# Optimization experiments

Hardware: AMD Instinct MI355X
Metric: run time of the kernel (lower is better)

## Reference

```python
import jax, jax.numpy as jnp
import numpy as np

HEADS = 8
EPS = 1e-5

def setup_inputs() -> dict:
    key = jax.random.key(0)
    ks = jax.random.split(key, 4)
    B, S, N, C = 1, 256, 384, 512
    msa = jax.random.normal(ks[0], (B, S, N, C), dtype=jnp.float32)
    mask = jnp.ones((B, S), dtype=jnp.int32)
    Wqkv = jax.random.normal(ks[1], (3 * C, C), dtype=jnp.float32) * (C ** -0.5)
    bqkv = jnp.zeros((3 * C,), dtype=jnp.float32)
    Wout = jax.random.normal(ks[2], (C, C), dtype=jnp.float32) * (C ** -0.5)
    bout = jnp.zeros((C,), dtype=jnp.float32)
    gamma = jnp.ones((C,), dtype=jnp.float32)
    beta = jnp.zeros((C,), dtype=jnp.float32)
    return {"msa": msa, "mask": mask, "Wqkv": Wqkv, "bqkv": bqkv,
            "Wout": Wout, "bout": bout, "gamma": gamma, "beta": beta}

def reference(msa, mask, Wqkv, bqkv, Wout, bout, gamma, beta):
    B, S, N, C = msa.shape
    H = HEADS
    Dh = C // H
    scale = Dh ** -0.5
    msa_t = jnp.transpose(msa, (0, 2, 1, 3))            # [B,N,S,C]
    qkv = msa_t @ Wqkv.T + bqkv                          # [B,N,S,3C]
    qkv = qkv.reshape(B, N, S, 3, H, Dh)
    q, k, v = qkv[..., 0, :, :], qkv[..., 1, :, :], qkv[..., 2, :, :]  # [B,N,S,H,Dh]
    attn = jnp.einsum('bnshc,bnthc->bhst', q, k) * scale  # reduce over N and head-dim
    attn = jnp.where(mask[:, None, None, :] == 0, -1e9, attn)
    attn = jax.nn.softmax(attn, axis=-1)                 # [B,H,S,S]
    out = jnp.einsum('bhst,bnthc->bnshc', attn, v).reshape(B, N, S, C)
    out = jnp.transpose(out, (0, 2, 1, 3))               # [B,S,N,C]
    out = out @ Wout.T + bout
    x = msa + out
    mu = jnp.mean(x, axis=-1, keepdims=True)
    var = jnp.mean((x - mu) ** 2, axis=-1, keepdims=True)
    return (x - mu) * jax.lax.rsqrt(var + EPS) * gamma + beta
```

## Files before the change

kernel.cpp:

```cpp
#include <hip/hip_runtime.h>

#define S_ 256
#define N_ 384
#define C_ 512
#define H_ 8
#define R_ (N_*S_)
#define SPLITK 32
#define NPK (N_/SPLITK)

typedef _Float16 f16;
typedef _Float16 f16x8 __attribute__((ext_vector_type(8)));
typedef float f32x4 __attribute__((ext_vector_type(4)));

#define MFMA16(a,b,c) __builtin_amdgcn_mfma_f32_16x16x32_f16(a,b,c,0,0,0)

typedef __attribute__((address_space(3))) unsigned int as3_u32;
typedef __attribute__((address_space(1))) const unsigned int as1_u32;

__device__ __forceinline__ void gl_lds16(const void* g, void* l) {
    __builtin_amdgcn_global_load_lds((as1_u32*)(unsigned long long)g,
                                     (as3_u32*)(unsigned long long)l, 16, 0, 0);
}

__device__ __forceinline__ int swz_off(int row, int g) {
    return row*64 + (((g) ^ (row & 7)) << 3);
}

__device__ __forceinline__ void stage_tile32(const f16* __restrict__ Ab,
                                             const f16* __restrict__ Bb,
                                             int stride, f16* As_, f16* Bs_,
                                             int tid, int wid) {
#pragma unroll
    for (int i = 0; i < 2; ++i) {
        int id = (i << 8) + tid;
        int row = id >> 2;
        int g = (id & 3) ^ ((row >> 1) & 3);
        int lofs = ((i << 8) + (wid << 6)) << 4;
        gl_lds16(Ab + row * stride + (g << 3), (char*)As_ + lofs);
        gl_lds16(Bb + row * stride + (g << 3), (char*)Bs_ + lofs);
    }
}

__device__ __forceinline__ void frag_mma32(const f16* As_, const f16* Bs_,
                                           int lane, int wr, int wc, f32x4 acc[4][4]) {
    int kg = lane >> 4;
    f16x8 af[4], bf[4];
#pragma unroll
    for (int m = 0; m < 4; ++m) {
        int row = wr + (m << 4) + (lane & 15);
        af[m] = *(const f16x8*)&As_[row * 32 + ((kg ^ ((row >> 1) & 3)) << 3)];
    }
#pragma unroll
    for (int j = 0; j < 4; ++j) {
        int row = wc + (j << 4) + (lane & 15);
        bf[j] = *(const f16x8*)&Bs_[row * 32 + ((kg ^ ((row >> 1) & 3)) << 3)];
    }
#pragma unroll
    for (int m = 0; m < 4; ++m)
#pragma unroll
        for (int j = 0; j < 4; ++j)
            acc[m][j] = MFMA16(af[m], bf[j], acc[m][j]);
}

__device__ __forceinline__ void frag_mma64(const f16* As_, const f16* Bs_,
                                           int lane, int wr, int wc, f32x4 acc[4][4]) {
#pragma unroll
    for (int ks = 0; ks < 64; ks += 32) {
        int kg = (ks >> 3) + (lane >> 4);
        f16x8 af[4], bf[4];
#pragma unroll
        for (int m = 0; m < 4; ++m)
            af[m] = *(const f16x8*)&As_[swz_off(wr + (m << 4) + (lane & 15), kg)];
#pragma unroll
        for (int j = 0; j < 4; ++j)
            bf[j] = *(const f16x8*)&Bs_[swz_off(wc + (j << 4) + (lane & 15), kg)];
#pragma unroll
        for (int m = 0; m < 4; ++m)
#pragma unroll
            for (int j = 0; j < 4; ++j)
                acc[m][j] = MFMA16(af[m], bf[j], acc[m][j]);
    }
}

__global__ __launch_bounds__(256) void k_prep(const float* __restrict__ Wqkv,
                                              const float* __restrict__ Wout,
                                              f16* __restrict__ Wq16, f16* __restrict__ Wo16) {
    int i = blockIdx.x * 256 + threadIdx.x;
    if (i < 1536 * C_) Wq16[i] = (f16)Wqkv[i];
    if (i < C_ * C_)   Wo16[i] = (f16)Wout[i];
}

__global__ __launch_bounds__(256) void k_cast(const float* __restrict__ msa,
                                              f16* __restrict__ msaT) {
    int t = blockIdx.x * 256 + threadIdx.x;
    int r = t >> 6, cg = t & 63;
    int n = r >> 8, s = r & 255;
    const float* src = msa + (s * N_ + n) * C_ + (cg << 3);
    float4 lo = *(const float4*)src;
    float4 hi = *(const float4*)(src + 4);
    f16x8 v;
    v[0]=(f16)lo.x; v[1]=(f16)lo.y; v[2]=(f16)lo.z; v[3]=(f16)lo.w;
    v[4]=(f16)hi.x; v[5]=(f16)hi.y; v[6]=(f16)hi.z; v[7]=(f16)hi.w;
    *(f16x8*)(msaT + r * C_ + (cg << 3)) = v;
}

__global__ __launch_bounds__(256) void k_qkv(const f16* __restrict__ msaT,
                                             const f16* __restrict__ W,
                                             const float* __restrict__ bqkv,
                                             f16* __restrict__ qk,
                                             f16* __restrict__ vT) {
    int wg = (blockIdx.x & 7) * 1152 + (blockIdx.x >> 3);
    int bx = wg / 12, by = wg % 12;
    int j0 = by << 7;
    int tid = threadIdx.x, lane = tid & 63, wid = tid >> 6;
    int wr = (wid >> 1) << 6, wc = (wid & 1) << 6;
    __shared__ f16 SH[16384];
    const f16* Abase = msaT + (bx << 7) * C_;
    const f16* Bbase = W + j0 * C_;
    f32x4 acc[4][4] = {};
    stage_tile32(Abase, Bbase, C_, SH, SH + 8192, tid, wid);
    __syncthreads();
    for (int t = 0; t < 16; ++t) {
        int cur = t & 1;
        if (t < 15)
            stage_tile32(Abase + ((t + 1) << 5), Bbase + ((t + 1) << 5), C_,
                         SH + ((cur ^ 1) << 12), SH + 8192 + ((cur ^ 1) << 12), tid, wid);
        frag_mma32(SH + (cur << 12), SH + 8192 + (cur << 12), lane, wr, wc, acc);
        __syncthreads();
    }
    if (by < 8) {
#pragma unroll
        for (int p = 0; p < 2; ++p) {
            __syncthreads();
#pragma unroll
            for (int mm = 0; mm < 2; ++mm) {
                int m = 2 * p + mm;
                int rl = (m << 4) + ((lane >> 4) << 2);
                int lrow = (wr >> 1) + rl - (p << 5);
#pragma unroll
                for (int j = 0; j < 4; ++j) {
                    int col = wc + (j << 4) + (lane & 15);
                    float bv = bqkv[j0 + col];
#pragma unroll
                    for (int q = 0; q < 4; ++q)
                        SH[(lrow + q) * 136 + col] = (f16)(acc[m][j][q] + bv);
                }
            }
            __syncthreads();
#pragma unroll
            for (int i = 0; i < 4; ++i) {
                int u = tid + (i << 8);
                int lrow = u >> 4, seg = u & 15;
                int grow = (bx << 7) + ((lrow >> 5) << 6) + (p << 5) + (lrow & 31);
                *(f16x8*)(qk + grow * 1024 + j0 + (seg << 3)) =
                    *(const f16x8*)&SH[lrow * 136 + (seg << 3)];
            }
        }
    } else {
        int n = bx >> 1, t0g = (bx & 1) << 7;
#pragma unroll
        for (int p = 0; p < 2; ++p) {
            __syncthreads();
#pragma unroll
            for (int m = 0; m < 4; ++m) {
                int rl = wr + (m << 4) + ((lane >> 4) << 2);
#pragma unroll
                for (int jj = 0; jj < 2; ++jj) {
                    int j = 2 * p + jj;
                    int col = wc + (j << 4) + (lane & 15);
                    int lcol = (col & 31) + ((col >> 6) << 5);
                    float bv = bqkv[1024 + (by - 8) * 128 + col];
#pragma unroll
                    for (int q = 0; q < 4; ++q)
                        SH[lcol * 136 + rl + q] = (f16)(acc[m][j][q] + bv);
                }
            }
            __syncthreads();
#pragma unroll
            for (int i = 0; i < 4; ++i) {
                int u = tid + (i << 8);
                int lcol = u >> 4, seg = u & 15;
                int col = (lcol & 31) + (p << 5) + ((lcol >> 5) << 6);
                int jg = (by - 8) * 128 + col;
                *(f16x8*)(vT + ((n * H_ + (jg >> 6)) * 64 + (jg & 63)) * S_ + t0g + (seg << 3)) =
                    *(const f16x8*)&SH[lcol * 136 + (seg << 3)];
            }
        }
    }
}

__global__ __launch_bounds__(256) void k_logits(const f16* __restrict__ qk,
                                                float* __restrict__ logP) {
    int wg = (blockIdx.x & 7) * 128 + (blockIdx.x >> 3);
    int sk = wg >> 5, rem = wg & 31, h = rem >> 2, sb = (rem >> 1) & 1, tb = rem & 1;
    int s0 = sb << 7, t0 = tb << 7, n0 = sk * NPK;
    int tid = threadIdx.x, lane = tid & 63, wid = tid >> 6;
    int wr = (wid >> 1) << 6, wc = (wid & 1) << 6;
    __shared__ f16 SH[16384];
    const f16* Aroot = qk + s0 * 1024 + (h << 6);
    const f16* Broot = qk + t0 * 1024 + 512 + (h << 6);
    f32x4 acc[4][4] = {};
    stage_tile32(Aroot + n0 * S_ * 1024, Broot + n0 * S_ * 1024, 1024,
                 SH, SH + 8192, tid, wid);
    __syncthreads();
    for (int t = 0; t < 2 * NPK; ++t) {
        int cur = t & 1;
        if (t < 2 * NPK - 1) {
            int tn = t + 1;
            int n = n0 + (tn >> 1), dh = (tn & 1) << 5;
            stage_tile32(Aroot + n * S_ * 1024 + dh, Broot + n * S_ * 1024 + dh, 1024,
                         SH + ((cur ^ 1) << 12), SH + 8192 + ((cur ^ 1) << 12), tid, wid);
        }
        frag_mma32(SH + (cur << 12), SH + 8192 + (cur << 12), lane, wr, wc, acc);
        __syncthreads();
    }
#pragma unroll
    for (int m = 0; m < 4; ++m) {
        int rloc = wr + (m << 4) + ((lane >> 4) << 2);
#pragma unroll
        for (int j = 0; j < 4; ++j) {
            int tc = t0 + wc + (j << 4) + (lane & 15);
#pragma unroll
            for (int q = 0; q < 4; ++q)
                logP[((sk * H_ + h) * S_ + s0 + rloc + q) * S_ + tc] = acc[m][j][q];
        }
    }
}

__global__ __launch_bounds__(256) void k_softmax(const float* __restrict__ logP,
                                                 const int* __restrict__ mask,
                                                 f16* __restrict__ attn) {
    int hs = blockIdx.x;
    int t = threadIdx.x, lane = t & 63, wid = t >> 6;
    float v = 0.f;
#pragma unroll
    for (int sk = 0; sk < SPLITK; ++sk)
        v += logP[(sk * H_ * S_ + hs) * S_ + t];
    v *= 0.125f;
    if (mask[t] == 0) v = -1e9f;
    __shared__ float redm[4], reds[4];
    float m_ = v;
    for (int o = 32; o > 0; o >>= 1) m_ = fmaxf(m_, __shfl_xor(m_, o));
    if (lane == 0) redm[wid] = m_;
    __syncthreads();
    float bm = fmaxf(fmaxf(redm[0], redm[1]), fmaxf(redm[2], redm[3]));
    float e = __expf(v - bm);
    float s_ = e;
    for (int o = 32; o > 0; o >>= 1) s_ += __shfl_xor(s_, o);
    if (lane == 0) reds[wid] = s_;
    __syncthreads();
    float tot = reds[0] + reds[1] + reds[2] + reds[3];
    attn[hs * S_ + t] = (f16)(e / tot);
}

__global__ __launch_bounds__(256) void k_pv(const f16* __restrict__ attn,
                                            const f16* __restrict__ vT,
                                            f16* __restrict__ attn_out) {
    int n = blockIdx.x >> 3, h = blockIdx.x & 7;
    int tid = threadIdx.x, lane = tid & 63, wid = tid >> 6;
    __shared__ f16 SH[20480];
    f16* As_ = SH;
    f16* Bs_ = SH + 16384;
    f32x4 acc[4][4] = {};
    const f16* Ab = attn + h * S_ * S_;
    const f16* Bb = vT + (n * H_ + h) * 64 * S_;
    for (int tt = 0; tt < 4; ++tt) {
        int t0 = tt << 6;
        __syncthreads();
#pragma unroll
        for (int i = 0; i < 8; ++i) {
            int id = (i << 8) + tid;
            int row = id >> 3, g = (id & 7) ^ (row & 7);
            int lofs = ((i << 8) + (wid << 6)) << 4;
            gl_lds16(Ab + row * S_ + t0 + (g << 3), (char*)As_ + lofs);
        }
#pragma unroll
        for (int i = 0; i < 2; ++i) {
            int id = (i << 8) + tid;
            int row = id >> 3, g = (id & 7) ^ (row & 7);
            int lofs = ((i << 8) + (wid << 6)) << 4;
            gl_lds16(Bb + row * S_ + t0 + (g << 3), (char*)Bs_ + lofs);
        }
        __syncthreads();
        frag_mma64(As_, Bs_, lane, wid << 6, 0, acc);
    }
#pragma unroll
    for (int p = 0; p < 2; ++p) {
        __syncthreads();
#pragma unroll
        for (int mm = 0; mm < 2; ++mm) {
            int m = 2 * p + mm;
            int rl = ((m & 1) << 4) + ((lane >> 4) << 2);
            int lrow = (wid << 5) + rl;
#pragma unroll
            for (int j = 0; j < 4; ++j) {
                int d = (j << 4) + (lane & 15);
#pragma unroll
                for (int q = 0; q < 4; ++q)
                    SH[(lrow + q) * 72 + d] = (f16)acc[m][j][q];
            }
        }
        __syncthreads();
#pragma unroll
        for (int i = 0; i < 4; ++i) {
            int u = tid + (i << 8);
            int row = u >> 3, seg = u & 7;
            int s = ((row >> 5) << 6) + (p << 5) + (row & 31);
            *(f16x8*)(attn_out + (n * S_ + s) * C_ + (h << 6) + (seg << 3)) =
                *(const f16x8*)&SH[row * 72 + (seg << 3)];
        }
    }
}

__global__ __launch_bounds__(512) void k_out_ln(const f16* __restrict__ attn_out,
                                                const f16* __restrict__ Wo,
                                                const float* __restrict__ bout,
                                                const f16* __restrict__ msaT,
                                                const float* __restrict__ gamma,
                                                const float* __restrict__ beta,
                                                float* __restrict__ out) {
    int r0 = blockIdx.x << 6;
    int n = r0 >> 8, s0 = r0 & 255;
    int tid = threadIdx.x, lane = tid & 63, wid = tid >> 6;
    __shared__ f16 SH[36864];
    f16* As_ = SH;
    f16* Bs_ = SH + 4096;
    __shared__ float redS[8][64], redQ[8][64], muS[64], rsS[64];
    f32x4 acc[4][4] = {};
    for (int kt = 0; kt < 8; ++kt) {
        int c0 = kt << 6;
        __syncthreads();
        {
            int row = tid >> 3, g = (tid & 7) ^ (row & 7);
            int lofs = (wid << 6) << 4;
            gl_lds16(attn_out + (r0 + row) * C_ + c0 + (g << 3), (char*)As_ + lofs);
        }
#pragma unroll
        for (int i = 0; i < 8; ++i) {
            int id = (i << 9) + tid;
            int row = id >> 3, g = (id & 7) ^ (row & 7);
            int lofs = ((i << 9) + (wid << 6)) << 4;
            gl_lds16(Wo + row * C_ + c0 + (g << 3), (char*)Bs_ + lofs);
        }
        __syncthreads();
        frag_mma64(As_, Bs_, lane, 0, wid << 6, acc);
    }
    float psum[4][4] = {}, psq[4][4] = {};
#pragma unroll
    for (int m = 0; m < 4; ++m)
#pragma unroll
        for (int j = 0; j < 4; ++j) {
            int c = (wid << 6) + (j << 4) + (lane & 15);
            float bj = bout[c];
#pragma unroll
            for (int q = 0; q < 4; ++q) {
                int rl = (m << 4) + ((lane >> 4) << 2) + q;
                float x = acc[m][j][q] + bj + (float)msaT[(r0 + rl) * C_ + c];
                acc[m][j][q] = x;
                psum[m][q] += x;
                psq[m][q] += x * x;
            }
        }
#pragma unroll
    for (int m = 0; m < 4; ++m)
#pragma unroll
        for (int q = 0; q < 4; ++q)
            for (int o = 1; o < 16; o <<= 1) {
                psum[m][q] += __shfl_xor(psum[m][q], o);
                psq[m][q]  += __shfl_xor(psq[m][q], o);
            }
    if ((lane & 15) == 0) {
#pragma unroll
        for (int m = 0; m < 4; ++m)
#pragma unroll
            for (int q = 0; q < 4; ++q) {
                int rl = (m << 4) + ((lane >> 4) << 2) + q;
                redS[wid][rl] = psum[m][q];
                redQ[wid][rl] = psq[m][q];
            }
    }
    __syncthreads();
    if (tid < 64) {
        float t1 = 0.f, t2 = 0.f;
#pragma unroll
        for (int w = 0; w < 8; ++w) { t1 += redS[w][tid]; t2 += redQ[w][tid]; }
        float mu = t1 * (1.0f / 512.0f);
        float var = t2 * (1.0f / 512.0f) - mu * mu;
        muS[tid] = mu;
        rsS[tid] = rsqrtf(var + 1e-5f);
    }
    __syncthreads();
#pragma unroll
    for (int m = 0; m < 4; ++m)
#pragma unroll
        for (int j = 0; j < 4; ++j) {
            int c = (wid << 6) + (j << 4) + (lane & 15);
            float g = gamma[c], bb = beta[c];
#pragma unroll
            for (int q = 0; q < 4; ++q) {
                int rl = (m << 4) + ((lane >> 4) << 2) + q;
                int s = s0 + rl;
                float y = (acc[m][j][q] - muS[rl]) * rsS[rl] * g + bb;
                out[(s * N_ + n) * C_ + c] = y;
            }
        }
}

extern "C" void kernel_launch(void* const* d_in, const int* in_sizes, int n_in,
                              void* d_out, int out_size, void* d_ws, size_t ws_size,
                              hipStream_t stream) {
    const float* msa   = (const float*)d_in[0];
    const int*   mask  = (const int*)d_in[1];
    const float* Wqkv  = (const float*)d_in[2];
    const float* bqkv  = (const float*)d_in[3];
    const float* Wout  = (const float*)d_in[4];
    const float* bout  = (const float*)d_in[5];
    const float* gamma = (const float*)d_in[6];
    const float* beta  = (const float*)d_in[7];
    float* out = (float*)d_out;
    char* ws = (char*)d_ws;

    f16*   qk   = (f16*)(ws);
    f16*   vT   = (f16*)(ws + 201326592);
    f16*   msaT = (f16*)(ws + 301989888);
    f16*   attn = (f16*)(ws + 402653184);
    f16*   Wq16 = (f16*)(ws + 403701760);
    f16*   Wo16 = (f16*)(ws + 405274624);
    float* logP = out;
    f16*   attn_out = qk;

    k_prep<<<dim3(3072), dim3(256), 0, stream>>>(Wqkv, Wout, Wq16, Wo16);
    k_cast<<<dim3(24576), dim3(256), 0, stream>>>(msa, msaT);
    k_qkv<<<dim3(9216), dim3(256), 0, stream>>>(msaT, Wq16, bqkv, qk, vT);
    k_logits<<<dim3(1024), dim3(256), 0, stream>>>(qk, logP);
    k_softmax<<<dim3(2048), dim3(256), 0, stream>>>(logP, mask, attn);
    k_pv<<<dim3(3072), dim3(256), 0, stream>>>(attn, vT, attn_out);
    k_out_ln<<<dim3(1536), dim3(512), 0, stream>>>(attn_out, Wo16, bout, msaT, gamma, beta, out);
}
```

Measured before the change: 628.5 us.

## Use 512-thread blocks and BK=64 tiles in QKV and logits GEMMs

```diff
diff --git a/kernel.cpp b/kernel.cpp
--- a/kernel.cpp
+++ b/kernel.cpp
@@ -26,40 +26,38 @@
     return row*64 + (((g) ^ (row & 7)) << 3);
 }
 
-__device__ __forceinline__ void stage_tile32(const f16* __restrict__ Ab,
-                                             const f16* __restrict__ Bb,
-                                             int stride, f16* As_, f16* Bs_,
-                                             int tid, int wid) {
+__device__ __forceinline__ void stage8(const f16* __restrict__ Ab,
+                                       const f16* __restrict__ Bb,
+                                       int stride, f16* As_, f16* Bs_,
+                                       int tid, int wid) {
 #pragma unroll
     for (int i = 0; i < 2; ++i) {
-        int id = (i << 8) + tid;
-        int row = id >> 2;
-        int g = (id & 3) ^ ((row >> 1) & 3);
-        int lofs = ((i << 8) + (wid << 6)) << 4;
+        int id = (i << 9) + tid;
+        int row = id >> 3, g = (id & 7) ^ (row & 7);
+        int lofs = ((i << 9) + (wid << 6)) << 4;
         gl_lds16(Ab + row * stride + (g << 3), (char*)As_ + lofs);
         gl_lds16(Bb + row * stride + (g << 3), (char*)Bs_ + lofs);
     }
 }
 
-__device__ __forceinline__ void frag_mma32(const f16* As_, const f16* Bs_,
-                                           int lane, int wr, int wc, f32x4 acc[4][4]) {
-    int kg = lane >> 4;
-    f16x8 af[4], bf[4];
-#pragma unroll
-    for (int m = 0; m < 4; ++m) {
-        int row = wr + (m << 4) + (lane & 15);
-        af[m] = *(const f16x8*)&As_[row * 32 + ((kg ^ ((row >> 1) & 3)) << 3)];
-    }
-#pragma unroll
-    for (int j = 0; j < 4; ++j) {
-        int row = wc + (j << 4) + (lane & 15);
-        bf[j] = *(const f16x8*)&Bs_[row * 32 + ((kg ^ ((row >> 1) & 3)) << 3)];
-    }
-#pragma unroll
-    for (int m = 0; m < 4; ++m)
-#pragma unroll
-        for (int j = 0; j < 4; ++j)
-            acc[m][j] = MFMA16(af[m], bf[j], acc[m][j]);
+__device__ __forceinline__ void mma8(const f16* As_, const f16* Bs_,
+                                     int lane, int wr, int wc, f32x4 acc[4][2]) {
+#pragma unroll
+    for (int ks = 0; ks < 64; ks += 32) {
+        int kg = (ks >> 3) + (lane >> 4);
+        f16x8 af[4], bf[2];
+#pragma unroll
+        for (int m = 0; m < 4; ++m)
+            af[m] = *(const f16x8*)&As_[swz_off(wr + (m << 4) + (lane & 15), kg)];
+#pragma unroll
+        for (int j = 0; j < 2; ++j)
+            bf[j] = *(const f16x8*)&Bs_[swz_off(wc + (j << 4) + (lane & 15), kg)];
+#pragma unroll
+        for (int m = 0; m < 4; ++m)
+#pragma unroll
+            for (int j = 0; j < 2; ++j)
+                acc[m][j] = MFMA16(af[m], bf[j], acc[m][j]);
+    }
 }
 
 __device__ __forceinline__ void frag_mma64(const f16* As_, const f16* Bs_,
@@ -104,7 +102,7 @@
     *(f16x8*)(msaT + r * C_ + (cg << 3)) = v;
 }
 
-__global__ __launch_bounds__(256) void k_qkv(const f16* __restrict__ msaT,
+__global__ __launch_bounds__(512) void k_qkv(const f16* __restrict__ msaT,
                                              const f16* __restrict__ W,
                                              const float* __restrict__ bqkv,
                                              f16* __restrict__ qk,
@@ -113,116 +111,101 @@
     int bx = wg / 12, by = wg % 12;
     int j0 = by << 7;
     int tid = threadIdx.x, lane = tid & 63, wid = tid >> 6;
-    int wr = (wid >> 1) << 6, wc = (wid & 1) << 6;
-    __shared__ f16 SH[16384];
+    int wr = (wid >> 2) << 6, wc = (wid & 3) << 5;
+    __shared__ f16 SH[32768];
     const f16* Abase = msaT + (bx << 7) * C_;
     const f16* Bbase = W + j0 * C_;
-    f32x4 acc[4][4] = {};
-    stage_tile32(Abase, Bbase, C_, SH, SH + 8192, tid, wid);
-    __syncthreads();
-    for (int t = 0; t < 16; ++t) {
-        int cur = t & 1;
-        if (t < 15)
-            stage_tile32(Abase + ((t + 1) << 5), Bbase + ((t + 1) << 5), C_,
-                         SH + ((cur ^ 1) << 12), SH + 8192 + ((cur ^ 1) << 12), tid, wid);
-        frag_mma32(SH + (cur << 12), SH + 8192 + (cur << 12), lane, wr, wc, acc);
+    f32x4 acc[4][2] = {};
+    stage8(Abase, Bbase, C_, SH, SH + 8192, tid, wid);
+    __syncthreads();
+    for (int kt = 0; kt < 8; ++kt) {
+        int cur = kt & 1;
+        if (kt < 7)
+            stage8(Abase + ((kt + 1) << 6), Bbase + ((kt + 1) << 6), C_,
+                   SH + ((cur ^ 1) << 14), SH + 8192 + ((cur ^ 1) << 14), tid, wid);
+        mma8(SH + (cur << 14), SH + 8192 + (cur << 14), lane, wr, wc, acc);
         __syncthreads();
     }
     if (by < 8) {
 #pragma unroll
-        for (int p = 0; p < 2; ++p) {
-            __syncthreads();
-#pragma unroll
-            for (int mm = 0; mm < 2; ++mm) {
-                int m = 2 * p + mm;
-                int rl = (m << 4) + ((lane >> 4) << 2);
-                int lrow = (wr >> 1) + rl - (p << 5);
-#pragma unroll
-                for (int j = 0; j < 4; ++j) {
-                    int col = wc + (j << 4) + (lane & 15);
-                    float bv = bqkv[j0 + col];
-#pragma unroll
-                    for (int q = 0; q < 4; ++q)
-                        SH[(lrow + q) * 136 + col] = (f16)(acc[m][j][q] + bv);
-                }
-            }
-            __syncthreads();
-#pragma unroll
-            for (int i = 0; i < 4; ++i) {
-                int u = tid + (i << 8);
-                int lrow = u >> 4, seg = u & 15;
-                int grow = (bx << 7) + ((lrow >> 5) << 6) + (p << 5) + (lrow & 31);
-                *(f16x8*)(qk + grow * 1024 + j0 + (seg << 3)) =
-                    *(const f16x8*)&SH[lrow * 136 + (seg << 3)];
-            }
+        for (int m = 0; m < 4; ++m) {
+            int rl = wr + (m << 4) + ((lane >> 4) << 2);
+#pragma unroll
+            for (int j = 0; j < 2; ++j) {
+                int col = wc + (j << 4) + (lane & 15);
+                float bv = bqkv[j0 + col];
+#pragma unroll
+                for (int q = 0; q < 4; ++q)
+                    SH[(rl + q) * 140 + col] = (f16)(acc[m][j][q] + bv);
+            }
+        }
+        __syncthreads();
+#pragma unroll
+        for (int i = 0; i < 4; ++i) {
+            int u = (i << 9) + tid;
+            int row = u >> 4, seg = u & 15;
+            *(f16x8*)(qk + ((bx << 7) + row) * 1024 + j0 + (seg << 3)) =
+                *(const f16x8*)&SH[row * 140 + (seg << 3)];
         }
     } else {
         int n = bx >> 1, t0g = (bx & 1) << 7;
 #pragma unroll
-        for (int p = 0; p < 2; ++p) {
-            __syncthreads();
-#pragma unroll
-            for (int m = 0; m < 4; ++m) {
-                int rl = wr + (m << 4) + ((lane >> 4) << 2);
-#pragma unroll
-                for (int jj = 0; jj < 2; ++jj) {
-                    int j = 2 * p + jj;
-                    int col = wc + (j << 4) + (lane & 15);
-                    int lcol = (col & 31) + ((col >> 6) << 5);
-                    float bv = bqkv[1024 + (by - 8) * 128 + col];
-#pragma unroll
-                    for (int q = 0; q < 4; ++q)
-                        SH[lcol * 136 + rl + q] = (f16)(acc[m][j][q] + bv);
-                }
-            }
-            __syncthreads();
-#pragma unroll
-            for (int i = 0; i < 4; ++i) {
-                int u = tid + (i << 8);
-                int lcol = u >> 4, seg = u & 15;
-                int col = (lcol & 31) + (p << 5) + ((lcol >> 5) << 6);
-                int jg = (by - 8) * 128 + col;
-                *(f16x8*)(vT + ((n * H_ + (jg >> 6)) * 64 + (jg & 63)) * S_ + t0g + (seg << 3)) =
-                    *(const f16x8*)&SH[lcol * 136 + (seg << 3)];
-            }
-        }
-    }
-}
-
-__global__ __launch_bounds__(256) void k_logits(const f16* __restrict__ qk,
+        for (int m = 0; m < 4; ++m) {
+            int rl = wr + (m << 4) + ((lane >> 4) << 2);
+#pragma unroll
+            for (int j = 0; j < 2; ++j) {
+                int col = wc + (j << 4) + (lane & 15);
+                float bv = bqkv[1024 + ((by - 8) << 7) + col];
+#pragma unroll
+                for (int q = 0; q < 4; ++q)
+                    SH[col * 140 + rl + q] = (f16)(acc[m][j][q] + bv);
+            }
+        }
+        __syncthreads();
+#pragma unroll
+        for (int i = 0; i < 4; ++i) {
+            int u = (i << 9) + tid;
+            int lcol = u >> 4, seg = u & 15;
+            int jg = ((by - 8) << 7) + lcol;
+            *(f16x8*)(vT + ((n * H_ + (jg >> 6)) * 64 + (jg & 63)) * S_ + t0g + (seg << 3)) =
+                *(const f16x8*)&SH[lcol * 140 + (seg << 3)];
+        }
+    }
+}
+
+__global__ __launch_bounds__(512) void k_logits(const f16* __restrict__ qk,
                                                 float* __restrict__ logP) {
     int wg = (blockIdx.x & 7) * 128 + (blockIdx.x >> 3);
     int sk = wg >> 5, rem = wg & 31, h = rem >> 2, sb = (rem >> 1) & 1, tb = rem & 1;
     int s0 = sb << 7, t0 = tb << 7, n0 = sk * NPK;
     int tid = threadIdx.x, lane = tid & 63, wid = tid >> 6;
-    int wr = (wid >> 1) << 6, wc = (wid & 1) << 6;
-    __shared__ f16 SH[16384];
+    int wr = (wid >> 2) << 6, wc = (wid & 3) << 5;
+    __shared__ f16 SH[32768];
     const f16* Aroot = qk + s0 * 1024 + (h << 6);
     const f16* Broot = qk + t0 * 1024 + 512 + (h << 6);
-    f32x4 acc[4][4] = {};
-    stage_tile32(Aroot + n0 * S_ * 1024, Broot + n0 * S_ * 1024, 1024,
-                 SH, SH + 8192, tid, wid);
-    __syncthreads();
-    for (int t = 0; t < 2 * NPK; ++t) {
+    f32x4 acc[4][2] = {};
+    stage8(Aroot + n0 * S_ * 1024, Broot + n0 * S_ * 1024, 1024,
+           SH, SH + 8192, tid, wid);
+    __syncthreads();
+    for (int t = 0; t < NPK; ++t) {
         int cur = t & 1;
-        if (t < 2 * NPK - 1) {
-            int tn = t + 1;
-            int n = n0 + (tn >> 1), dh = (tn & 1) << 5;
-            stage_tile32(Aroot + n * S_ * 1024 + dh, Broot + n * S_ * 1024 + dh, 1024,
-                         SH + ((cur ^ 1) << 12), SH + 8192 + ((cur ^ 1) << 12), tid, wid);
-        }
-        frag_mma32(SH + (cur << 12), SH + 8192 + (cur << 12), lane, wr, wc, acc);
+        if (t < NPK - 1) {
+            int n = n0 + t + 1;
+            stage8(Aroot + n * S_ * 1024, Broot + n * S_ * 1024, 1024,
+                   SH + ((cur ^ 1) << 14), SH + 8192 + ((cur ^ 1) << 14), tid, wid);
+        }
+        mma8(SH + (cur << 14), SH + 8192 + (cur << 14), lane, wr, wc, acc);
         __syncthreads();
     }
 #pragma unroll
     for (int m = 0; m < 4; ++m) {
-        int rloc = wr + (m << 4) + ((lane >> 4) << 2);
-#pragma unroll
-        for (int j = 0; j < 4; ++j) {
+        int rl = wr + (m << 4) + ((lane >> 4) << 2);
+#pragma unroll
+        for (int j = 0; j < 2; ++j) {
             int tc = t0 + wc + (j << 4) + (lane & 15);
 #pragma unroll
             for (int q = 0; q < 4; ++q)
-                logP[((sk * H_ + h) * S_ + s0 + rloc + q) * S_ + tc] = acc[m][j][q];
+                logP[((sk * H_ + h) * S_ + s0 + rl + q) * S_ + tc] = acc[m][j][q];
         }
     }
 }
@@ -297,7 +280,7 @@
                 int d = (j << 4) + (lane & 15);
 #pragma unroll
                 for (int q = 0; q < 4; ++q)
-                    SH[(lrow + q) * 72 + d] = (f16)acc[m][j][q];
+                    SH[(lrow + q) * 140 + d] = (f16)acc[m][j][q];
             }
         }
         __syncthreads();
@@ -307,7 +290,7 @@
             int row = u >> 3, seg = u & 7;
             int s = ((row >> 5) << 6) + (p << 5) + (row & 31);
             *(f16x8*)(attn_out + (n * S_ + s) * C_ + (h << 6) + (seg << 3)) =
-                *(const f16x8*)&SH[row * 72 + (seg << 3)];
+                *(const f16x8*)&SH[row * 140 + (seg << 3)];
         }
     }
 }
@@ -431,8 +414,8 @@
 
     k_prep<<<dim3(3072), dim3(256), 0, stream>>>(Wqkv, Wout, Wq16, Wo16);
     k_cast<<<dim3(24576), dim3(256), 0, stream>>>(msa, msaT);
-    k_qkv<<<dim3(9216), dim3(256), 0, stream>>>(msaT, Wq16, bqkv, qk, vT);
-    k_logits<<<dim3(1024), dim3(256), 0, stream>>>(qk, logP);
+    k_qkv<<<dim3(9216), dim3(512), 0, stream>>>(msaT, Wq16, bqkv, qk, vT);
+    k_logits<<<dim3(1024), dim3(512), 0, stream>>>(qk, logP);
     k_softmax<<<dim3(2048), dim3(256), 0, stream>>>(logP, mask, attn);
     k_pv<<<dim3(3072), dim3(256), 0, stream>>>(attn, vT, attn_out);
     k_out_ln<<<dim3(1536), dim3(512), 0, stream>>>(attn_out, Wo16, bout, msaT, gamma, beta, out);
```

New measurement: 580.2 us. 1.08x faster.
